# Performance work log

Measured on AMD Instinct MI355X. Metric: run time of the kernel, lower is better.

The kernel has to match this reference:

```python
import jax, jax.numpy as jnp
import numpy as np

# dims: batch, cdd_size, his_size, signal_length, embedding_dim, filter_num, top-k, levels, vocab
B, CDD, HIS, S, E, F, K, L, VOCAB = 32, 5, 50, 20, 300, 150, 30, 3, 50000


def _conv1d(x, w, b, d):
    # x: [N, C_in, S], w: [C_out, C_in, 3], 'same' length via padding=d, dilation=d
    y = jax.lax.conv_general_dilated(x, w, (1,), [(d, d)], rhs_dilation=(d,),
                                     dimension_numbers=('NCW', 'OIW', 'NCW'))
    return y + b[None, :, None]


def _conv3d(x, w, b):
    # x: [N, C_in, D, H, W], padding 1 on all spatial dims
    y = jax.lax.conv_general_dilated(x, w, (1, 1, 1), [(1, 1)] * 3,
                                     dimension_numbers=('NCDHW', 'OIDHW', 'NCDHW'))
    return y + b[None, :, None, None, None]


def _maxpool3(x):
    return jax.lax.reduce_window(x, -jnp.inf, jax.lax.max,
                                 (1, 1, 3, 3, 3), (1, 1, 3, 3, 3), 'VALID')


def setup_inputs() -> dict:
    key = jax.random.key(0)
    ks = jax.random.split(key, 12)
    n = lambda k, s, sc=0.05: jax.random.normal(k, s, dtype=jnp.float32) * sc
    return {
        'candidate_title': jax.random.randint(ks[0], (B, CDD, S), 0, VOCAB),
        'clicked_title': jax.random.randint(ks[1], (B, HIS, S), 0, VOCAB),
        'his_mask': jnp.zeros((B, HIS, 1), dtype=bool),
        'embedding': n(ks[2], (VOCAB, E), 0.1),
        'w1': n(ks[3], (F, E, 3)), 'b1': jnp.zeros((F,), jnp.float32),
        'w2': n(ks[4], (F, F, 3)), 'b2': jnp.zeros((F,), jnp.float32),
        'w3': n(ks[5], (F, F, 3)), 'b3': jnp.zeros((F,), jnp.float32),
        'ln_w': jnp.ones((F,), jnp.float32), 'ln_b': jnp.zeros((F,), jnp.float32),
        'q_words': n(ks[6], (1, F), 1.0), 'q_levels': n(ks[7], (1, F), 1.0),
        'c3d_w1': n(ks[8], (32, L, 3, 3, 3)), 'c3d_b1': jnp.zeros((32,), jnp.float32),
        'c3d_w2': n(ks[9], (16, 32, 3, 3, 3)), 'c3d_b2': jnp.zeros((16,), jnp.float32),
        'ltr_w': n(ks[10], (1, 192)), 'ltr_b': jnp.zeros((1,), jnp.float32),
    }


def reference(candidate_title, clicked_title, his_mask, embedding,
              w1, b1, w2, b2, w3, b3, ln_w, ln_b, q_words, q_levels,
              c3d_w1, c3d_b1, c3d_w2, c3d_b2, ltr_w, ltr_b):
    def ln(x):
        m = x.mean(-1, keepdims=True)
        v = x.var(-1, keepdims=True)  # biased var, matches torch LayerNorm
        return (x - m) / jnp.sqrt(v + 1e-5) * ln_w + ln_b

    scale_e = jnp.sqrt(jnp.float32(E))  # NOTE: original divides by sqrt(embedding_dim)

    def encode(ids):
        nn = ids.shape[1]
        x = embedding[ids].reshape(-1, S, E).transpose(0, 2, 1)  # [N, E, S] (dropout = identity at eval)
        d1 = ln(_conv1d(x, w1, b1, 1).transpose(0, 2, 1))                     # [N, S, F]
        d2 = ln(_conv1d(d1.transpose(0, 2, 1), w2, b2, 2).transpose(0, 2, 1))
        d3 = ln(_conv1d(d2.transpose(0, 2, 1), w3, b3, 3).transpose(0, 2, 1))
        dil = jnp.stack([jax.nn.relu(d1), jax.nn.relu(d2), jax.nn.relu(d3)], axis=2)  # [N, S, L, F]
        dil = dil.reshape(B, nn, S, L, F)
        # level attention with query_levels
        lw = jax.nn.softmax(jnp.einsum('bnslf,f->bnsl', dil, q_levels[0]) / scale_e, axis=-1)
        wf = jnp.einsum('bnsl,bnslf->bnsf', lw, dil)
        # word attention with query_words
        ww = jax.nn.softmax(jnp.einsum('bnsf,f->bns', wf, q_words[0]) / scale_e, axis=-1)
        reprs = jnp.einsum('bns,bnsf->bnf', ww, wf)
        return dil, reprs

    cdd_emb, cdd_repr = encode(candidate_title)   # [B,CDD,S,L,F], [B,CDD,F]
    his_emb, his_repr = encode(clicked_title)     # [B,HIS,S,L,F], [B,HIS,F]

    # news-level attention -> top-k one-hot gating (gather of history news)
    scores = jnp.einsum('bcf,bhf->bch', cdd_repr, his_repr)
    scores = jnp.where(his_mask.transpose(0, 2, 1), -jnp.inf, scores)
    attn = jax.nn.softmax(scores, axis=-1)
    _, idx = jax.lax.top_k(attn, K)                                  # [B,CDD,K]
    his_act = his_emb[jnp.arange(B)[:, None, None], idx]             # [B,CDD,K,S,L,F]

    # fusion tensor: per-level word-word interaction maps
    cdd_t = cdd_emb.transpose(0, 1, 3, 2, 4)       # [B,CDD,L,S,F]
    his_t = his_act.transpose(0, 1, 2, 4, 3, 5)    # [B,CDD,K,L,S,F]
    fusion = jnp.einsum('bclsf,bckltf->bcklst', cdd_t, his_t) / jnp.sqrt(jnp.float32(F))
    fusion = fusion.reshape(B * CDD, K, L, S, S).transpose(0, 2, 1, 3, 4)  # [B*CDD, L, K, S, S]

    h = _maxpool3(jax.nn.relu(_conv3d(fusion, c3d_w1, c3d_b1)))
    h = _maxpool3(jax.nn.relu(_conv3d(h, c3d_w2, c3d_b2)))
    feat = h.reshape(B, CDD, -1)                   # [B, CDD, 192]
    score = jnp.einsum('bcd,d->bc', feat, ltr_w[0]) + ltr_b[0]
    return jax.nn.log_softmax(score, axis=-1)
```

## Files before the change

kernel.cpp:

```cpp
#include <hip/hip_runtime.h>
#include <hip/hip_bf16.h>

#define NB   32
#define NCDD 5
#define NHIS 50
#define SS   20
#define EE   300
#define FF   150
#define KK   30
#define LL   3
#define NSEQ (NB*NCDD + NB*NHIS)
#define NCD  (NB*NCDD)
#define NROW (NSEQ*SS)
#define CONVGRID (NROW/64)

typedef unsigned short u16;
typedef __attribute__((ext_vector_type(8))) short bf16x8;
typedef __attribute__((ext_vector_type(4))) float f32x4;
typedef __attribute__((ext_vector_type(4))) unsigned int u32x4;

__device__ __forceinline__ float b2f(u16 v) {
    union { unsigned int u; float f; } c; c.u = ((unsigned int)v) << 16; return c.f;
}
__device__ __forceinline__ u16 f2b(float f) {
    union { float f; unsigned int u; } c; c.f = f;
    unsigned int r = c.u + 0x7FFF + ((c.u >> 16) & 1);
    return (u16)(r >> 16);
}
__device__ __forceinline__ float ldf(const void* p, size_t i, int isbf) {
    return isbf ? b2f(((const u16*)p)[i]) : ((const float*)p)[i];
}
__device__ __forceinline__ float dget(const float* d, size_t i) {
    unsigned int u = ((const unsigned int*)d)[i];
    return b2f((u16)(u & 0xffffu)) + b2f((u16)(u >> 16));
}
__device__ __forceinline__ bf16x8 ld_frag8(const u16* p) {
    uint2 q0 = *(const uint2*)(p);
    uint2 q1 = *(const uint2*)(p + 4);
    u32x4 t; t.x = q0.x; t.y = q0.y; t.z = q1.x; t.w = q1.y;
    return __builtin_bit_cast(bf16x8, t);
}

__global__ void detect_dtype(const u16* lnw_raw, int* flag) {
    if (threadIdx.x == 0)
        flag[0] = (lnw_raw[0] == 0x3F80 && lnw_raw[1] == 0x3F80) ? 1 : 0;
}

struct CJob { const void* src; float* dst; int n; };
struct CJobs { CJob j[13]; };

__global__ __launch_bounds__(256) void convert_many(CJobs jobs, const int* flagp) {
    int isbf = flagp[0];
    CJob job = jobs.j[blockIdx.x];
    for (int i = threadIdx.x; i < job.n; i += 256) job.dst[i] = ldf(job.src, i, isbf);
}

__global__ __launch_bounds__(256) void repack_wb(const void* w, const int* flagp,
                                                 u16* outh, u16* outl,
                                                 int CIN, int KP, int CV) {
    int isbf = flagp[0];
    int i = blockIdx.x*256 + threadIdx.x;
    if (i >= 160*3*KP) return;
    int g = i % KP; int r = i / KP; int tap = r % 3; int f = r / 3;
    float v = 0.f;
    if (f < FF && g < CV) v = ldf(w, ((size_t)f*CIN + g)*3 + tap, isbf);
    u16 hi = f2b(v);
    u16 lo = f2b(v - b2f(hi));
    size_t o = (size_t)f*(3*KP) + (size_t)tap*KP + g;
    outh[o] = hi; outl[o] = lo;
}

__global__ __launch_bounds__(256) void repack_w2(const void* w, const int* flagp,
                                                 u16* outh, u16* outl) {
    int isbf = flagp[0];
    int i = blockIdx.x*256 + threadIdx.x;
    if (i >= 16*864) return;
    int ic = i & 31; int r = i >> 5; int tap = r % 27; int oc = r / 27;
    float v = ldf(w, ((size_t)oc*32 + ic)*27 + tap, isbf);
    u16 hi = f2b(v); u16 lo = f2b(v - b2f(hi));
    size_t o = (size_t)oc*864 + tap*32 + ic;
    outh[o] = hi; outl[o] = lo;
}

template<int STAGE>
__global__ __launch_bounds__(256, 2) void conv_mfma(const int* __restrict__ flagp,
        const int* __restrict__ cand, const int* __restrict__ clik,
        const void* __restrict__ emb,
        const unsigned int* __restrict__ dprev,
        const u16* __restrict__ wh, const u16* __restrict__ wl,
        const float* __restrict__ bias,
        const float* __restrict__ lnw, const float* __restrict__ lnb,
        unsigned int* __restrict__ dout)
{
    constexpr int KC  = 32;
    constexpr int PAD = 40;
    constexpr int KT  = (STAGE == 0) ? 960 : 480;
    constexpr int NC  = KT / KC;
    constexpr int DIL = (STAGE == 1) ? 2 : 3;
    constexpr int ASZ = 64*PAD, BSZ = 160*PAD;
    constexpr int STG = (2*ASZ + 2*BSZ)*2;
    constexpr int SMB = (STG > 64*164*4) ? STG : 64*164*4;
    __shared__ __align__(16) char smem[SMB];
    u16* Ah = (u16*)smem;
    u16* Al = Ah + ASZ;
    u16* Bh = Al + ASZ;
    u16* Bl = Bh + BSZ;

    const int tid  = threadIdx.x;
    const int row0 = blockIdx.x * 64;
    const int lane = tid & 63, wid = tid >> 6;
    const int wm = wid >> 1, wn = wid & 1;
    const int lr = lane & 15, lk = lane >> 4;
    const int isbf = flagp[0];

    const int arow = tid >> 2, aseg = tid & 3;
    const int grow = row0 + arow;
    const int an   = grow / 20;
    const int as   = grow - an*20;
    int aid[3];
    if constexpr (STAGE == 0) {
        #pragma unroll
        for (int t = 0; t < 3; ++t) {
            int w = as + t - 1;
            aid[t] = ((unsigned)w < 20u) ? ((an < NCD) ? cand[an*SS + w] : clik[(an - NCD)*SS + w])
                                         : -1;
        }
    }

    float xa[8];
    uint4 ra32[2];
    uint4 rb[5];

    auto LOADG = [&](int c) {
        if constexpr (STAGE == 0) {
            int tap = c / 10;
            int e0  = (c - tap*10)*32 + aseg*8;
            int id  = aid[tap];
            float4 x0 = {0.f,0.f,0.f,0.f}, x1 = {0.f,0.f,0.f,0.f};
            if (id >= 0) {
                if (!isbf) {
                    const float* ep = (const float*)emb + (size_t)id*EE + e0;
                    if (e0 < EE)     x0 = *(const float4*)ep;
                    if (e0 + 4 < EE) x1 = *(const float4*)(ep + 4);
                } else {
                    const u16* ep = (const u16*)emb + (size_t)id*EE + e0;
                    float t[8];
                    #pragma unroll
                    for (int j = 0; j < 8; ++j) t[j] = (e0 + j < EE) ? b2f(ep[j]) : 0.f;
                    x0.x=t[0]; x0.y=t[1]; x0.z=t[2]; x0.w=t[3];
                    x1.x=t[4]; x1.y=t[5]; x1.z=t[6]; x1.w=t[7];
                }
            }
            xa[0]=x0.x; xa[1]=x0.y; xa[2]=x0.z; xa[3]=x0.w;
            xa[4]=x1.x; xa[5]=x1.y; xa[6]=x1.z; xa[7]=x1.w;
        } else {
            int tap = c / 5;
            int f0  = (c - tap*5)*32;
            int word = as + DIL*(tap - 1);
            int gbase = f0 + aseg*8;
            ra32[0].x=ra32[0].y=ra32[0].z=ra32[0].w=0u;
            ra32[1].x=ra32[1].y=ra32[1].z=ra32[1].w=0u;
            if ((unsigned)word < 20u && gbase < FF) {
                const unsigned int* p = dprev + (size_t)(an*SS + word)*FF + gbase;
                uint2 q0 = *(const uint2*)(p);
                uint2 q1 = *(const uint2*)(p + 2);
                uint2 q2 = *(const uint2*)(p + 4);
                uint2 q3 = *(const uint2*)(p + 6);
                ra32[0].x = q0.x; ra32[0].y = q0.y; ra32[0].z = q1.x; ra32[0].w = q1.y;
                ra32[1].x = q2.x; ra32[1].y = q2.y; ra32[1].z = q3.x; ra32[1].w = q3.y;
                if (gbase + 7 >= FF) {
                    if (gbase + 1 >= FF) ra32[0].y = 0u;
                    if (gbase + 2 >= FF) ra32[0].z = 0u;
                    if (gbase + 3 >= FF) ra32[0].w = 0u;
                    if (gbase + 4 >= FF) ra32[1].x = 0u;
                    if (gbase + 5 >= FF) ra32[1].y = 0u;
                    if (gbase + 6 >= FF) ra32[1].z = 0u;
                    ra32[1].w = 0u;
                }
            }
        }
        #pragma unroll
        for (int j = 0; j < 5; ++j) {
            int item = tid + j*256;
            const u16* wp = (item < 640) ? wh : wl;
            int rem  = (item < 640) ? item : item - 640;
            rb[j] = *(const uint4*)(wp + (size_t)(rem >> 2)*KT + c*KC + (rem & 3)*8);
        }
    };

    auto WRITE = [&]() {
        uint4 h, l;
        if constexpr (STAGE == 0) {
            u16 hh[8], lo[8];
            #pragma unroll
            for (int j = 0; j < 8; ++j) {
                hh[j] = f2b(xa[j]);
                lo[j] = f2b(xa[j] - b2f(hh[j]));
            }
            h.x = hh[0] | ((unsigned)hh[1] << 16); h.y = hh[2] | ((unsigned)hh[3] << 16);
            h.z = hh[4] | ((unsigned)hh[5] << 16); h.w = hh[6] | ((unsigned)hh[7] << 16);
            l.x = lo[0] | ((unsigned)lo[1] << 16); l.y = lo[2] | ((unsigned)lo[3] << 16);
            l.z = lo[4] | ((unsigned)lo[5] << 16); l.w = lo[6] | ((unsigned)lo[7] << 16);
        } else {
            h.x = (ra32[0].x & 0xffffu) | (ra32[0].y << 16);
            h.y = (ra32[0].z & 0xffffu) | (ra32[0].w << 16);
            h.z = (ra32[1].x & 0xffffu) | (ra32[1].y << 16);
            h.w = (ra32[1].z & 0xffffu) | (ra32[1].w << 16);
            l.x = (ra32[0].x >> 16) | (ra32[0].y & 0xffff0000u);
            l.y = (ra32[0].z >> 16) | (ra32[0].w & 0xffff0000u);
            l.z = (ra32[1].x >> 16) | (ra32[1].y & 0xffff0000u);
            l.w = (ra32[1].z >> 16) | (ra32[1].w & 0xffff0000u);
        }
        *(uint4*)(Ah + arow*PAD + aseg*8) = h;
        *(uint4*)(Al + arow*PAD + aseg*8) = l;
        #pragma unroll
        for (int j = 0; j < 5; ++j) {
            int item = tid + j*256;
            u16* bp = (item < 640) ? Bh : Bl;
            int rem = (item < 640) ? item : item - 640;
            *(uint4*)(bp + (rem >> 2)*PAD + (rem & 3)*8) = rb[j];
        }
    };

    f32x4 acc[2][5];
    #pragma unroll
    for (int mf = 0; mf < 2; ++mf)
        #pragma unroll
        for (int nf = 0; nf < 5; ++nf)
            acc[mf][nf] = (f32x4){0.f,0.f,0.f,0.f};

    auto COMPUTE = [&]() {
        bf16x8 fah[2], fal[2], fbh[5], fbl[5];
        #pragma unroll
        for (int mf = 0; mf < 2; ++mf) {
            fah[mf] = *(const bf16x8*)(Ah + (wm*32 + mf*16 + lr)*PAD + lk*8);
            fal[mf] = *(const bf16x8*)(Al + (wm*32 + mf*16 + lr)*PAD + lk*8);
        }
        #pragma unroll
        for (int nf = 0; nf < 5; ++nf) {
            fbh[nf] = *(const bf16x8*)(Bh + (wn*80 + nf*16 + lr)*PAD + lk*8);
            fbl[nf] = *(const bf16x8*)(Bl + (wn*80 + nf*16 + lr)*PAD + lk*8);
        }
        #pragma unroll
        for (int mf = 0; mf < 2; ++mf)
            #pragma unroll
            for (int nf = 0; nf < 5; ++nf)
                acc[mf][nf] = __builtin_amdgcn_mfma_f32_16x16x32_bf16(fah[mf], fbh[nf], acc[mf][nf], 0, 0, 0);
        #pragma unroll
        for (int mf = 0; mf < 2; ++mf)
            #pragma unroll
            for (int nf = 0; nf < 5; ++nf)
                acc[mf][nf] = __builtin_amdgcn_mfma_f32_16x16x32_bf16(fah[mf], fbl[nf], acc[mf][nf], 0, 0, 0);
        #pragma unroll
        for (int mf = 0; mf < 2; ++mf)
            #pragma unroll
            for (int nf = 0; nf < 5; ++nf)
                acc[mf][nf] = __builtin_amdgcn_mfma_f32_16x16x32_bf16(fal[mf], fbh[nf], acc[mf][nf], 0, 0, 0);
    };

    LOADG(0); WRITE();
    for (int c = 0; c < NC; ++c) {
        if (c + 1 < NC) LOADG(c + 1);
        __syncthreads();
        COMPUTE();
        __syncthreads();
        if (c + 1 < NC) WRITE();
    }

    float* outb = (float*)smem;
    #pragma unroll
    for (int mf = 0; mf < 2; ++mf)
        #pragma unroll
        for (int nf = 0; nf < 5; ++nf)
            #pragma unroll
            for (int r = 0; r < 4; ++r)
                outb[(wm*32 + mf*16 + lk*4 + r)*164 + wn*80 + nf*16 + lr] = acc[mf][nf][r];
    __syncthreads();

    for (int rl = wid*16; rl < wid*16 + 16; ++rl) {
        float vv[3]; float sum = 0.f, sq = 0.f;
        #pragma unroll
        for (int j = 0; j < 3; ++j) {
            int f = lane + j*64;
            float v = 0.f;
            if (f < FF) v = outb[rl*164 + f] + bias[f];
            vv[j] = v; sum += v; sq += v*v;
        }
        #pragma unroll
        for (int off = 32; off; off >>= 1) { sum += __shfl_down(sum, off); sq += __shfl_down(sq, off); }
        sum = __shfl(sum, 0); sq = __shfl(sq, 0);
        float m = sum / FF, var = sq / FF - m*m, inv = rsqrtf(var + 1e-5f);
        #pragma unroll
        for (int j = 0; j < 3; ++j) {
            int f = lane + j*64;
            if (f < FF) {
                float v = (vv[j] - m) * inv * lnw[f] + lnb[f];
                u16 hi = f2b(v);
                unsigned int lo = (unsigned int)f2b(v - b2f(hi));
                dout[(size_t)(row0 + rl)*FF + f] = (unsigned int)hi | (lo << 16);
            }
        }
    }
}

__global__ __launch_bounds__(256) void lvwd_attn(const float* d1, const float* d2, const float* d3,
                                                 const float* ql, const float* qw, float* reprs) {
    __shared__ float wfs[SS*FF];
    __shared__ float scs[SS];
    int n = blockIdx.x, tid = threadIdx.x;
    int wave = tid >> 6, lane = tid & 63;
    for (int s = wave; s < SS; s += 4) {
        size_t base = ((size_t)n*SS + s) * FF;
        float v[3][3];
        float dt[3] = {0.f, 0.f, 0.f};
        #pragma unroll
        for (int j = 0; j < 3; ++j) {
            int f = lane + j*64;
            float q = (f < FF) ? ql[f] : 0.f;
            float x0 = (f < FF) ? fmaxf(dget(d1, base+f), 0.f) : 0.f;
            float x1 = (f < FF) ? fmaxf(dget(d2, base+f), 0.f) : 0.f;
            float x2 = (f < FF) ? fmaxf(dget(d3, base+f), 0.f) : 0.f;
            v[0][j] = x0; v[1][j] = x1; v[2][j] = x2;
            dt[0] += x0*q; dt[1] += x1*q; dt[2] += x2*q;
        }
        #pragma unroll
        for (int off = 32; off; off >>= 1) {
            dt[0] += __shfl_xor(dt[0], off);
            dt[1] += __shfl_xor(dt[1], off);
            dt[2] += __shfl_xor(dt[2], off);
        }
        const float sc = 0.057735026918962584f;
        float a0 = dt[0]*sc, a1 = dt[1]*sc, a2 = dt[2]*sc;
        float mx = fmaxf(a0, fmaxf(a1, a2));
        float e0 = expf(a0-mx), e1 = expf(a1-mx), e2 = expf(a2-mx);
        float den = e0+e1+e2;
        float l0 = e0/den, l1 = e1/den, l2 = e2/den;
        #pragma unroll
        for (int j = 0; j < 3; ++j) {
            int f = lane + j*64;
            if (f < FF) wfs[s*FF + f] = l0*v[0][j] + l1*v[1][j] + l2*v[2][j];
        }
    }
    __syncthreads();
    if (wave == 0) {
        if (lane < SS) {
            float a = 0.f;
            for (int f = 0; f < FF; ++f) a += wfs[lane*FF + f]*qw[f];
            scs[lane] = a * 0.057735026918962584f;
        }
        float mx = -1e30f;
        #pragma unroll
        for (int s = 0; s < SS; ++s) mx = fmaxf(mx, scs[s]);
        float ww[SS]; float den = 0.f;
        #pragma unroll
        for (int s = 0; s < SS; ++s) { ww[s] = expf(scs[s]-mx); den += ww[s]; }
        float inv = 1.f/den;
        for (int f = lane; f < FF; f += 64) {
            float a = 0.f;
            #pragma unroll
            for (int s = 0; s < SS; ++s) a += ww[s]*wfs[s*FF + f];
            reprs[(size_t)n*FF + f] = a*inv;
        }
    }
}

__global__ __launch_bounds__(256) void score_kernel(const float* reprs, const unsigned char* mask,
                                                    float* scores) {
    int i = blockIdx.x*256 + threadIdx.x;
    if (i >= NB*NCDD*NHIS) return;
    int b = i/(NCDD*NHIS); int r = i%(NCDD*NHIS); int h = r%NHIS; int c = r/NHIS;
    const float* cr = reprs + (size_t)(b*NCDD + c)*FF;
    const float* hr = reprs + (size_t)(NCD + b*NHIS + h)*FF;
    float a = 0.f;
    for (int f = 0; f < FF; ++f) a += cr[f]*hr[f];
    if (mask[b*NHIS + h]) a = -1e30f;
    scores[i] = a;
}

__global__ __launch_bounds__(64) void topk_kernel(const float* scores, int* idx) {
    int i = blockIdx.x*64 + threadIdx.x;
    if (i >= NB*NCDD) return;
    float sc[NHIS];
    const float* sp = scores + i*NHIS;
    for (int h = 0; h < NHIS; ++h) sc[h] = sp[h];
    for (int k = 0; k < KK; ++k) {
        int best = 0; float bv = -1e38f;
        for (int h = 0; h < NHIS; ++h) { if (sc[h] > bv) { bv = sc[h]; best = h; } }
        idx[i*KK + k] = best;
        sc[best] = -1e38f;
    }
}

__global__ __launch_bounds__(256) void fusion_kernel(const float* d1, const float* d2, const float* d3,
                                                     const int* idx, float* fus) {
    constexpr int RS  = 168;
    constexpr int TSZ = 32*RS;
    __shared__ __align__(16) u16 smem[4*TSZ];
    u16* Ah = smem;
    u16* Al = smem + TSZ;
    u16* Hh = smem + 2*TSZ;
    u16* Hl = smem + 3*TSZ;
    int blk = blockIdx.x;
    int k = blk % KK; int r2 = blk / KK; int l = r2 % LL; int bc = r2 / LL;
    int b = bc / NCDD;
    int nh = NCD + b*NHIS + idx[bc*KK + k];
    const float* dl = (l == 0) ? d1 : ((l == 1) ? d2 : d3);
    const unsigned int* Ap = (const unsigned int*)dl + (size_t)bc*SS*FF;
    const unsigned int* Hp = (const unsigned int*)dl + (size_t)nh*SS*FF;
    int tid = threadIdx.x;
    for (int i = tid; i < 4*TSZ/8; i += 256)
        *(uint4*)(smem + (size_t)i*8) = (uint4){0u,0u,0u,0u};
    __syncthreads();
    for (int item = tid; item < 760; item += 256) {
        int side = item >= 380;
        int rem  = side ? item - 380 : item;
        int row  = rem / 19, f0 = (rem - row*19)*8;
        const unsigned int* p = (side ? Hp : Ap) + row*FF + f0;
        unsigned int q[8];
        #pragma unroll
        for (int j = 0; j < 8; j += 2) {
            uint2 t2 = {0u, 0u};
            if (f0 + j < FF) t2 = *(const uint2*)(p + j);
            q[j] = t2.x; q[j+1] = t2.y;
        }
        unsigned int hh[8], ll[8];
        #pragma unroll
        for (int j = 0; j < 8; ++j) {
            unsigned int u = q[j];
            float f = b2f((u16)(u & 0xffffu)) + b2f((u16)(u >> 16));
            int keep = (f > 0.f);
            hh[j] = keep ? (u & 0xffffu) : 0u;
            ll[j] = keep ? (u >> 16)     : 0u;
        }
        uint4 h, lo;
        h.x  = hh[0] | (hh[1] << 16); h.y  = hh[2] | (hh[3] << 16);
        h.z  = hh[4] | (hh[5] << 16); h.w  = hh[6] | (hh[7] << 16);
        lo.x = ll[0] | (ll[1] << 16); lo.y = ll[2] | (ll[3] << 16);
        lo.z = ll[4] | (ll[5] << 16); lo.w = ll[6] | (ll[7] << 16);
        u16* dh = (side ? Hh : Ah) + row*RS + f0;
        u16* dL = (side ? Hl : Al) + row*RS + f0;
        *(uint4*)dh = h;
        *(uint4*)dL = lo;
    }
    __syncthreads();
    const int lane = tid & 63, wid = tid >> 6;
    const int wm = wid >> 1, wn = wid & 1;
    const int lr = lane & 15, lk = lane >> 4;
    f32x4 acc = {0.f, 0.f, 0.f, 0.f};
    #pragma unroll
    for (int c = 0; c < 5; ++c) {
        bf16x8 fah = *(const bf16x8*)(Ah + (wm*16 + lr)*RS + c*32 + lk*8);
        bf16x8 fal = *(const bf16x8*)(Al + (wm*16 + lr)*RS + c*32 + lk*8);
        bf16x8 fbh = *(const bf16x8*)(Hh + (wn*16 + lr)*RS + c*32 + lk*8);
        bf16x8 fbl = *(const bf16x8*)(Hl + (wn*16 + lr)*RS + c*32 + lk*8);
        acc = __builtin_amdgcn_mfma_f32_16x16x32_bf16(fah, fbh, acc, 0, 0, 0);
        acc = __builtin_amdgcn_mfma_f32_16x16x32_bf16(fah, fbl, acc, 0, 0, 0);
        acc = __builtin_amdgcn_mfma_f32_16x16x32_bf16(fal, fbh, acc, 0, 0, 0);
    }
    #pragma unroll
    for (int r = 0; r < 4; ++r) {
        int s = wm*16 + lk*4 + r, t = wn*16 + lr;
        if (s < SS && t < SS)
            fus[(size_t)blk*400 + s*20 + t] = acc[r] * 0.08164965809277261f;
    }
}

__global__ __launch_bounds__(256) void c3d1_kernel(const float* __restrict__ fus,
                                                   const float* __restrict__ w,
                                                   const float* __restrict__ bias,
                                                   unsigned int* __restrict__ h1p) {
    __shared__ float Sin[3*5*22*22];
    __shared__ float Wls[32*81];
    int blk = blockIdx.x;
    int dz = blk % 10; int bc = blk / 10;
    int tid = threadIdx.x;
    for (int i = tid; i < 32*81; i += 256) Wls[i] = w[i];
    int z0 = dz*3 - 1;
    for (int i = tid; i < 3*5*22*22; i += 256) {
        int x = i % 22; int r = i / 22;
        int y = r % 22; r /= 22;
        int zl = r % 5; int ic = r / 5;
        int zz = z0 + zl, yy = y - 1, xx = x - 1;
        float v = 0.f;
        if ((unsigned)zz < 30u && (unsigned)yy < 20u && (unsigned)xx < 20u)
            v = fus[((size_t)(bc*3 + ic)*30 + zz)*400 + yy*20 + xx];
        Sin[i] = v;
    }
    __syncthreads();
    for (int item = tid; item < 1152; item += 256) {
        int oc = item & 31; int dydx = item >> 5;
        int dy = dydx / 6, dx = dydx % 6;
        float acc[27];
        #pragma unroll
        for (int j = 0; j < 27; ++j) acc[j] = 0.f;
        int ybase = dy*3, xbase = dx*3;
        for (int ic = 0; ic < 3; ++ic) {
            #pragma unroll
            for (int zl = 0; zl < 5; ++zl) {
                float p[5][5];
                const float* sp = &Sin[((ic*5 + zl)*22 + ybase)*22 + xbase];
                #pragma unroll
                for (int yy = 0; yy < 5; ++yy)
                    #pragma unroll
                    for (int xx = 0; xx < 5; ++xx) p[yy][xx] = sp[yy*22 + xx];
                #pragma unroll
                for (int pz = 0; pz < 3; ++pz) {
                    int kz = zl - pz;
                    if (kz < 0 || kz > 2) continue;
                    const float* wv = &Wls[oc*81 + ic*27 + kz*9];
                    #pragma unroll
                    for (int ky = 0; ky < 3; ++ky)
                    #pragma unroll
                    for (int kx = 0; kx < 3; ++kx) {
                        float wgt = wv[ky*3 + kx];
                        #pragma unroll
                        for (int py = 0; py < 3; ++py)
                        #pragma unroll
                        for (int px = 0; px < 3; ++px)
                            acc[pz*9 + py*3 + px] += p[py+ky][px+kx] * wgt;
                    }
                }
            }
        }
        float best = -1e30f;
        #pragma unroll
        for (int j = 0; j < 27; ++j) best = fmaxf(best, acc[j]);
        float v = fmaxf(best + bias[oc], 0.f);
        u16 hi = f2b(v);
        unsigned int lo = (unsigned int)f2b(v - b2f(hi));
        h1p[((size_t)(bc*10 + dz)*36 + dydx)*32 + oc] = (unsigned int)hi | (lo << 16);
    }
}

#define ARS 36
#define APL (36*ARS)
__global__ __launch_bounds__(256) void c3d2_kernel(const unsigned int* __restrict__ h1p,
                                                   const u16* __restrict__ wh,
                                                   const u16* __restrict__ wl,
                                                   const float* __restrict__ bias,
                                                   float* __restrict__ h2) {
    __shared__ __align__(16) u16 Ah[12*APL];
    __shared__ __align__(16) u16 Al[12*APL];
    int bc = blockIdx.x, tid = threadIdx.x;
    for (int i = tid; i < 2*APL; i += 256) {
        int a = (i < APL) ? i : (11*APL + i - APL);
        Ah[a] = 0; Al[a] = 0;
    }
    for (int i = tid; i < 10*36*32; i += 256) {
        int ic = i & 31; int r = i >> 5; int yx = r % 36; int z = r / 36;
        unsigned int u = h1p[(size_t)bc*11520 + i];
        int a = (z + 1)*APL + yx*ARS + ic;
        Ah[a] = (u16)(u & 0xffffu);
        Al[a] = (u16)(u >> 16);
    }
    __syncthreads();
    const int lane = tid & 63, wid = tid >> 6;
    const int lr = lane & 15, lk = lane >> 4;
    const int t0 = wid*6;
    int rr[6], rz[6], ry[6], rx[6];
    #pragma unroll
    for (int ti = 0; ti < 6; ++ti) {
        int r = (t0 + ti)*16 + lr;
        rr[ti] = r;
        int z = r / 36; int yx = r - z*36; int y = yx / 6;
        rz[ti] = z; ry[ti] = y; rx[ti] = yx - y*6;
    }
    f32x4 acc[6];
    #pragma unroll
    for (int ti = 0; ti < 6; ++ti) acc[ti] = (f32x4){0.f,0.f,0.f,0.f};
    for (int tap = 0; tap < 27; ++tap) {
        int kz = tap/9, kyx = tap - kz*9, ky = kyx/3, kx = kyx - ky*3;
        bf16x8 fbh = *(const bf16x8*)(wh + (size_t)lr*864 + tap*32 + lk*8);
        bf16x8 fbl = *(const bf16x8*)(wl + (size_t)lr*864 + tap*32 + lk*8);
        #pragma unroll
        for (int ti = 0; ti < 6; ++ti) {
            int yy = ry[ti] + ky - 1;
            int xx = rx[ti] + kx - 1;
            bool ok = (rr[ti] < 360) && ((unsigned)yy < 6u) && ((unsigned)xx < 6u);
            int a = ok ? ((rz[ti] + kz)*APL + (yy*6 + xx)*ARS + lk*8) : (lk*8);
            bf16x8 fah = ld_frag8(Ah + a);
            bf16x8 fal = ld_frag8(Al + a);
            acc[ti] = __builtin_amdgcn_mfma_f32_16x16x32_bf16(fah, fbh, acc[ti], 0, 0, 0);
            acc[ti] = __builtin_amdgcn_mfma_f32_16x16x32_bf16(fah, fbl, acc[ti], 0, 0, 0);
            acc[ti] = __builtin_amdgcn_mfma_f32_16x16x32_bf16(fal, fbh, acc[ti], 0, 0, 0);
        }
    }
    float b = bias[lr];
    #pragma unroll
    for (int ti = 0; ti < 6; ++ti) {
        #pragma unroll
        for (int r4 = 0; r4 < 4; ++r4) {
            int row = (t0 + ti)*16 + lk*4 + r4;
            if (row < 360)
                h2[((size_t)bc*16 + lr)*360 + row] = fmaxf(acc[ti][r4] + b, 0.f);
        }
    }
}

__global__ __launch_bounds__(256) void pool2_kernel(const float* h2, float* h2p) {
    int i = blockIdx.x*256 + threadIdx.x;
    if (i >= NCD*16*3*2*2) return;
    int dx = i % 2; int r = i/2;
    int dy = r % 2; r /= 2;
    int dz = r % 3; r /= 3;
    int oc = r % 16; r /= 16;
    int bc = r;
    const float* hp = h2 + ((size_t)bc*16 + oc)*360;
    float best = -1e30f;
    for (int pz = 0; pz < 3; ++pz)
    for (int py = 0; py < 3; ++py)
    for (int px = 0; px < 3; ++px) {
        int z = dz*3+pz, y = dy*3+py, x = dx*3+px;
        best = fmaxf(best, hp[(z*6 + y)*6 + x]);
    }
    h2p[i] = best;
}

__global__ __launch_bounds__(64) void ltr_kernel(const float* h2p, const float* lw,
                                                 const float* lb, float* sc) {
    int i = blockIdx.x*64 + threadIdx.x;
    if (i >= NB*NCDD) return;
    const float* f = h2p + (size_t)i*192;
    float a = lb[0];
    for (int d = 0; d < 192; ++d) a += f[d]*lw[d];
    sc[i] = a;
}

__global__ __launch_bounds__(64) void lsm_kernel(const float* sc, const int* flagp, void* out) {
    int b = threadIdx.x;
    if (b >= NB) return;
    int isbf = flagp[0];
    float v[NCDD]; float mx = -1e30f;
    #pragma unroll
    for (int c = 0; c < NCDD; ++c) { v[c] = sc[b*NCDD + c]; mx = fmaxf(mx, v[c]); }
    float den = 0.f;
    #pragma unroll
    for (int c = 0; c < NCDD; ++c) den += expf(v[c]-mx);
    float lse = mx + logf(den);
    #pragma unroll
    for (int c = 0; c < NCDD; ++c) {
        float o = v[c] - lse;
        if (isbf) ((u16*)out)[b*NCDD + c] = f2b(o);
        else      ((float*)out)[b*NCDD + c] = o;
    }
}

extern "C" void kernel_launch(void* const* d_in, const int* in_sizes, int n_in,
                              void* d_out, int out_size, void* d_ws, size_t ws_size,
                              hipStream_t stream) {
    const int* cand  = (const int*)d_in[0];
    const int* clik  = (const int*)d_in[1];
    const unsigned char* mask = (const unsigned char*)d_in[2];
    const void* emb  = d_in[3];
    const void* w1   = d_in[4];
    const void* b1   = d_in[5];
    const void* w2   = d_in[6];
    const void* b2   = d_in[7];
    const void* w3   = d_in[8];
    const void* b3   = d_in[9];
    const void* lnw  = d_in[10];
    const void* lnb  = d_in[11];
    const void* qw   = d_in[12];
    const void* ql   = d_in[13];
    const void* cw1  = d_in[14];
    const void* cb1  = d_in[15];
    const void* cw2  = d_in[16];
    const void* cb2  = d_in[17];
    const void* lw   = d_in[18];
    const void* lb   = d_in[19];

    char* wsb = (char*)d_ws;
    size_t off = 0;
    auto A = [&](size_t bytes) -> void* {
        void* p = wsb + off;
        off = (off + bytes + 255) & ~(size_t)255;
        return p;
    };
    int*   flag = (int*)A(4);
    float* b1f  = (float*)A(FF*4);
    float* b2f  = (float*)A(FF*4);
    float* b3f  = (float*)A(FF*4);
    float* lnwf = (float*)A(FF*4);
    float* lnbf = (float*)A(FF*4);
    float* qwf  = (float*)A(FF*4);
    float* qlf  = (float*)A(FF*4);
    float* c1w  = (float*)A(32*3*27*4);
    float* c1b  = (float*)A(32*4);
    float* c2w  = (float*)A(16*32*27*4);
    float* c2b  = (float*)A(16*4);
    float* lwf  = (float*)A(192*4);
    float* lbf  = (float*)A(4);
    u16*   wt1h = (u16*)A((size_t)160*960*2);
    u16*   wt1l = (u16*)A((size_t)160*960*2);
    u16*   wt2h = (u16*)A((size_t)160*480*2);
    u16*   wt2l = (u16*)A((size_t)160*480*2);
    u16*   wt3h = (u16*)A((size_t)160*480*2);
    u16*   wt3l = (u16*)A((size_t)160*480*2);
    u16*   w2ch = (u16*)A((size_t)16*864*2);
    u16*   w2cl = (u16*)A((size_t)16*864*2);
    float* d1   = (float*)A((size_t)NSEQ*SS*FF*4);
    float* d2   = (float*)A((size_t)NSEQ*SS*FF*4);
    float* d3   = (float*)A((size_t)NSEQ*SS*FF*4);
    float* fus  = (float*)A((size_t)NCD*LL*KK*SS*SS*4);
    float* reprs= (float*)A((size_t)NSEQ*FF*4);
    float* scb  = (float*)A((size_t)NB*NCDD*NHIS*4);
    int*   idx  = (int*)A((size_t)NB*NCDD*KK*4);
    unsigned int* h1p = (unsigned int*)d1;
    float* h2   = d2;
    float* h2p  = d3;
    float* fsc  = (float*)((char*)d3 + 256*1024);
    (void)ws_size; (void)in_sizes; (void)n_in; (void)out_size;

    detect_dtype<<<1, 64, 0, stream>>>((const u16*)lnw, flag);

    CJobs jobs;
    jobs.j[0]  = {b1,  b1f,  FF};
    jobs.j[1]  = {b2,  b2f,  FF};
    jobs.j[2]  = {b3,  b3f,  FF};
    jobs.j[3]  = {lnw, lnwf, FF};
    jobs.j[4]  = {lnb, lnbf, FF};
    jobs.j[5]  = {qw,  qwf,  FF};
    jobs.j[6]  = {ql,  qlf,  FF};
    jobs.j[7]  = {cw1, c1w,  32*3*27};
    jobs.j[8]  = {cb1, c1b,  32};
    jobs.j[9]  = {cw2, c2w,  16*32*27};
    jobs.j[10] = {cb2, c2b,  16};
    jobs.j[11] = {lw,  lwf,  192};
    jobs.j[12] = {lb,  lbf,  1};
    convert_many<<<13, 256, 0, stream>>>(jobs, flag);
    repack_wb<<<(160*960 + 255)/256, 256, 0, stream>>>(w1, flag, wt1h, wt1l, EE, 320, 300);
    repack_wb<<<(160*480 + 255)/256, 256, 0, stream>>>(w2, flag, wt2h, wt2l, FF, 160, 150);
    repack_wb<<<(160*480 + 255)/256, 256, 0, stream>>>(w3, flag, wt3h, wt3l, FF, 160, 150);
    repack_w2<<<(16*864 + 255)/256, 256, 0, stream>>>(cw2, flag, w2ch, w2cl);

    conv_mfma<0><<<CONVGRID, 256, 0, stream>>>(flag, cand, clik, emb, nullptr,
                                               wt1h, wt1l, b1f, lnwf, lnbf, (unsigned int*)d1);
    conv_mfma<1><<<CONVGRID, 256, 0, stream>>>(flag, cand, clik, emb, (const unsigned int*)d1,
                                               wt2h, wt2l, b2f, lnwf, lnbf, (unsigned int*)d2);
    conv_mfma<2><<<CONVGRID, 256, 0, stream>>>(flag, cand, clik, emb, (const unsigned int*)d2,
                                               wt3h, wt3l, b3f, lnwf, lnbf, (unsigned int*)d3);

    lvwd_attn<<<NSEQ, 256, 0, stream>>>(d1, d2, d3, qlf, qwf, reprs);
    score_kernel<<<(NB*NCDD*NHIS + 255)/256, 256, 0, stream>>>(reprs, mask, scb);
    topk_kernel<<<(NB*NCDD + 63)/64, 64, 0, stream>>>(scb, idx);
    fusion_kernel<<<NCD*LL*KK, 256, 0, stream>>>(d1, d2, d3, idx, fus);
    c3d1_kernel<<<NCD*10, 256, 0, stream>>>(fus, c1w, c1b, h1p);
    c3d2_kernel<<<NCD, 256, 0, stream>>>(h1p, w2ch, w2cl, c2b, h2);
    pool2_kernel<<<(NCD*16*3*2*2 + 255)/256, 256, 0, stream>>>(h2, h2p);
    ltr_kernel<<<(NB*NCDD + 63)/64, 64, 0, stream>>>(h2p, lwf, lbf, fsc);
    lsm_kernel<<<1, 64, 0, stream>>>(fsc, flag, d_out);
}
```

Before: 815.5 us.

## Rewrite first 3D conv as split-bf16 MFMA implicit GEMM with atomic maxpool

```diff
diff --git a/kernel.cpp b/kernel.cpp
--- a/kernel.cpp
+++ b/kernel.cpp
@@ -68,6 +68,21 @@
     u16 lo = f2b(v - b2f(hi));
     size_t o = (size_t)f*(3*KP) + (size_t)tap*KP + g;
     outh[o] = hi; outl[o] = lo;
+}
+
+__global__ __launch_bounds__(256) void repack_w1c(const void* w, const int* flagp,
+                                                  u16* outh, u16* outl) {
+    int isbf = flagp[0];
+    int i = blockIdx.x*256 + threadIdx.x;
+    if (i >= 3*32*32) return;
+    int k = i & 31; int oc = (i >> 5) & 31; int kx = i >> 10;
+    float v = 0.f;
+    if (k < 27) {
+        int kz = k / 9, r = k - kz*9, ky = r / 3, ic = r - ky*3;
+        v = ldf(w, ((((size_t)oc*3 + ic)*3 + kz)*3 + ky)*3 + kx, isbf);
+    }
+    u16 hi = f2b(v); u16 lo = f2b(v - b2f(hi));
+    outh[i] = hi; outl[i] = lo;
 }
 
 __global__ __launch_bounds__(256) void repack_w2(const void* w, const int* flagp,
@@ -465,70 +480,96 @@
     }
 }
 
-__global__ __launch_bounds__(256) void c3d1_kernel(const float* __restrict__ fus,
-                                                   const float* __restrict__ w,
-                                                   const float* __restrict__ bias,
-                                                   unsigned int* __restrict__ h1p) {
-    __shared__ float Sin[3*5*22*22];
-    __shared__ float Wls[32*81];
+#define C1RS 36
+__global__ __launch_bounds__(256) void c3d1_mfma(const float* __restrict__ fus,
+                                                 const u16* __restrict__ wh,
+                                                 const u16* __restrict__ wl,
+                                                 const float* __restrict__ bias,
+                                                 unsigned int* __restrict__ h1p) {
+    __shared__ __align__(16) u16 Ah[209*C1RS];
+    __shared__ __align__(16) u16 Al[209*C1RS];
+    __shared__ int mb[18*32];
     int blk = blockIdx.x;
-    int dz = blk % 10; int bc = blk / 10;
+    int yh = blk & 1; int r0 = blk >> 1; int g = r0 % 10; int bc = r0 / 10;
     int tid = threadIdx.x;
-    for (int i = tid; i < 32*81; i += 256) Wls[i] = w[i];
-    int z0 = dz*3 - 1;
-    for (int i = tid; i < 3*5*22*22; i += 256) {
-        int x = i % 22; int r = i / 22;
-        int y = r % 22; r /= 22;
-        int zl = r % 5; int ic = r / 5;
-        int zz = z0 + zl, yy = y - 1, xx = x - 1;
-        float v = 0.f;
-        if ((unsigned)zz < 30u && (unsigned)yy < 20u && (unsigned)xx < 20u)
-            v = fus[((size_t)(bc*3 + ic)*30 + zz)*400 + yy*20 + xx];
-        Sin[i] = v;
-    }
-    __syncthreads();
-    for (int item = tid; item < 1152; item += 256) {
-        int oc = item & 31; int dydx = item >> 5;
-        int dy = dydx / 6, dx = dydx % 6;
-        float acc[27];
-        #pragma unroll
-        for (int j = 0; j < 27; ++j) acc[j] = 0.f;
-        int ybase = dy*3, xbase = dx*3;
-        for (int ic = 0; ic < 3; ++ic) {
+    for (int i = tid; i < 18*32; i += 256) mb[i] = 0;
+    for (int i = tid; i < 209*C1RS; i += 256) { Ah[i] = 0; Al[i] = 0; }
+    const int lane = tid & 63, wid = tid >> 6;
+    const int lr = lane & 15, lk = lane >> 4;
+    const float b0 = bias[lr], b1 = bias[16 + lr];
+
+    for (int zi = 0; zi < 3; ++zi) {
+        int z = g*3 + zi;
+        __syncthreads();
+        for (int it = tid; it < 27*208; it += 256) {
+            int k = it / 208, p = it - k*208;
+            int kz = k / 9, r2 = k - kz*9, ky = r2 / 3, ic = r2 - ky*3;
+            int yp = p / 22, cx = p - yp*22;
+            int gy = yh*9 + yp + ky - 1;
+            int gx = cx - 1;
+            int zz = z + kz - 1;
+            float v = 0.f;
+            if (p < 198 && (unsigned)gy < 20u && (unsigned)gx < 20u && (unsigned)zz < 30u)
+                v = fus[((size_t)(bc*3 + ic)*30 + zz)*400 + gy*20 + gx];
+            u16 hi = f2b(v);
+            Ah[p*C1RS + k] = hi;
+            Al[p*C1RS + k] = f2b(v - b2f(hi));
+        }
+        __syncthreads();
+        f32x4 acc[4][2];
+        #pragma unroll
+        for (int fi = 0; fi < 4; ++fi) { acc[fi][0] = (f32x4){0,0,0,0}; acc[fi][1] = (f32x4){0,0,0,0}; }
+        #pragma unroll
+        for (int kx = 0; kx < 3; ++kx) {
+            bf16x8 bh0 = *(const bf16x8*)(wh + kx*1024 + lr*32 + lk*8);
+            bf16x8 bl0 = *(const bf16x8*)(wl + kx*1024 + lr*32 + lk*8);
+            bf16x8 bh1 = *(const bf16x8*)(wh + kx*1024 + (16 + lr)*32 + lk*8);
+            bf16x8 bl1 = *(const bf16x8*)(wl + kx*1024 + (16 + lr)*32 + lk*8);
             #pragma unroll
-            for (int zl = 0; zl < 5; ++zl) {
-                float p[5][5];
-                const float* sp = &Sin[((ic*5 + zl)*22 + ybase)*22 + xbase];
-                #pragma unroll
-                for (int yy = 0; yy < 5; ++yy)
-                    #pragma unroll
-                    for (int xx = 0; xx < 5; ++xx) p[yy][xx] = sp[yy*22 + xx];
-                #pragma unroll
-                for (int pz = 0; pz < 3; ++pz) {
-                    int kz = zl - pz;
-                    if (kz < 0 || kz > 2) continue;
-                    const float* wv = &Wls[oc*81 + ic*27 + kz*9];
-                    #pragma unroll
-                    for (int ky = 0; ky < 3; ++ky)
-                    #pragma unroll
-                    for (int kx = 0; kx < 3; ++kx) {
-                        float wgt = wv[ky*3 + kx];
-                        #pragma unroll
-                        for (int py = 0; py < 3; ++py)
-                        #pragma unroll
-                        for (int px = 0; px < 3; ++px)
-                            acc[pz*9 + py*3 + px] += p[py+ky][px+kx] * wgt;
-                    }
+            for (int fi = 0; fi < 4; ++fi) {
+                int frag = wid + fi*4;
+                if (frag >= 13) break;
+                int p = frag*16 + lr + (kx - 1);
+                int adr = (p < 0 ? 0 : p)*C1RS + lk*8;
+                bf16x8 ah = ld_frag8(Ah + adr);
+                bf16x8 al = ld_frag8(Al + adr);
+                acc[fi][0] = __builtin_amdgcn_mfma_f32_16x16x32_bf16(ah, bh0, acc[fi][0], 0, 0, 0);
+                acc[fi][0] = __builtin_amdgcn_mfma_f32_16x16x32_bf16(ah, bl0, acc[fi][0], 0, 0, 0);
+                acc[fi][0] = __builtin_amdgcn_mfma_f32_16x16x32_bf16(al, bh0, acc[fi][0], 0, 0, 0);
+                acc[fi][1] = __builtin_amdgcn_mfma_f32_16x16x32_bf16(ah, bh1, acc[fi][1], 0, 0, 0);
+                acc[fi][1] = __builtin_amdgcn_mfma_f32_16x16x32_bf16(ah, bl1, acc[fi][1], 0, 0, 0);
+                acc[fi][1] = __builtin_amdgcn_mfma_f32_16x16x32_bf16(al, bh1, acc[fi][1], 0, 0, 0);
+            }
+        }
+        #pragma unroll
+        for (int fi = 0; fi < 4; ++fi) {
+            int frag = wid + fi*4;
+            if (frag >= 13) break;
+            #pragma unroll
+            for (int r4 = 0; r4 < 4; ++r4) {
+                int p = frag*16 + lk*4 + r4;
+                if (p >= 198) continue;
+                int yp = p / 22, cx = p - yp*22;
+                int gx = cx - 1;
+                if ((unsigned)gx < 18u) {
+                    int cell = (yp/3)*6 + gx/3;
+                    float v0 = fmaxf(acc[fi][0][r4] + b0, 0.f);
+                    float v1 = fmaxf(acc[fi][1][r4] + b1, 0.f);
+                    atomicMax(&mb[cell*32 + lr],      __float_as_int(v0));
+                    atomicMax(&mb[cell*32 + 16 + lr], __float_as_int(v1));
                 }
             }
         }
-        float best = -1e30f;
-        #pragma unroll
-        for (int j = 0; j < 27; ++j) best = fmaxf(best, acc[j]);
-        float v = fmaxf(best + bias[oc], 0.f);
+    }
+    __syncthreads();
+    for (int i = tid; i < 18*32; i += 256) {
+        int oc = i & 31, cell = i >> 5;
+        int dyl = cell / 6, dx = cell - dyl*6;
+        int dydx = (yh*3 + dyl)*6 + dx;
+        float v = __int_as_float(mb[i]);
         u16 hi = f2b(v);
         unsigned int lo = (unsigned int)f2b(v - b2f(hi));
-        h1p[((size_t)(bc*10 + dz)*36 + dydx)*32 + oc] = (unsigned int)hi | (lo << 16);
+        h1p[((size_t)(bc*10 + g)*36 + dydx)*32 + oc] = (unsigned int)hi | (lo << 16);
     }
 }
 
@@ -696,6 +737,8 @@
     u16*   wt2l = (u16*)A((size_t)160*480*2);
     u16*   wt3h = (u16*)A((size_t)160*480*2);
     u16*   wt3l = (u16*)A((size_t)160*480*2);
+    u16*   w1ch = (u16*)A((size_t)3*32*32*2);
+    u16*   w1cl = (u16*)A((size_t)3*32*32*2);
     u16*   w2ch = (u16*)A((size_t)16*864*2);
     u16*   w2cl = (u16*)A((size_t)16*864*2);
     float* d1   = (float*)A((size_t)NSEQ*SS*FF*4);
@@ -731,6 +774,7 @@
     repack_wb<<<(160*960 + 255)/256, 256, 0, stream>>>(w1, flag, wt1h, wt1l, EE, 320, 300);
     repack_wb<<<(160*480 + 255)/256, 256, 0, stream>>>(w2, flag, wt2h, wt2l, FF, 160, 150);
     repack_wb<<<(160*480 + 255)/256, 256, 0, stream>>>(w3, flag, wt3h, wt3l, FF, 160, 150);
+    repack_w1c<<<(3*32*32 + 255)/256, 256, 0, stream>>>(cw1, flag, w1ch, w1cl);
     repack_w2<<<(16*864 + 255)/256, 256, 0, stream>>>(cw2, flag, w2ch, w2cl);
 
     conv_mfma<0><<<CONVGRID, 256, 0, stream>>>(flag, cand, clik, emb, nullptr,
@@ -744,7 +788,7 @@
     score_kernel<<<(NB*NCDD*NHIS + 255)/256, 256, 0, stream>>>(reprs, mask, scb);
     topk_kernel<<<(NB*NCDD + 63)/64, 64, 0, stream>>>(scb, idx);
     fusion_kernel<<<NCD*LL*KK, 256, 0, stream>>>(d1, d2, d3, idx, fus);
-    c3d1_kernel<<<NCD*10, 256, 0, stream>>>(fus, c1w, c1b, h1p);
+    c3d1_mfma<<<NCD*10*2, 256, 0, stream>>>(fus, w1ch, w1cl, c1b, h1p);
     c3d2_kernel<<<NCD, 256, 0, stream>>>(h1p, w2ch, w2cl, c2b, h2);
     pool2_kernel<<<(NCD*16*3*2*2 + 255)/256, 256, 0, stream>>>(h2, h2p);
     ltr_kernel<<<(NB*NCDD + 63)/64, 64, 0, stream>>>(h2p, lwf, lbf, fsc);
```

Result: no change. 828.2 us (+1.6%).
